# Kernel optimization log

Measured on AMD Instinct MI355X. Metric: run time of the kernel, lower is better.

Reference implementation:

```python
import jax, jax.numpy as jnp
import numpy as np

N = 8192          # number of nodes
E = 524288        # number of edges (avg degree 64)
D = 256           # latent_dim
NEG_FILL = -1e9   # torch.full fill value


def setup_inputs() -> dict:
    key = jax.random.key(0)
    k1, k2, k3, k4, k5, k6 = jax.random.split(key, 6)
    encoded = jax.random.normal(k1, (N, D), dtype=jnp.float32)
    h = jax.random.normal(k2, (N, D), dtype=jnp.float32)
    edge_index = jax.random.randint(k3, (2, E), 0, N, dtype=jnp.int64)
    edge_attr = jax.random.normal(k4, (E,), dtype=jnp.float32)
    # Linear weights (bias=False); stored as [in, out] for x @ W
    W1 = jax.random.normal(k5, (2 * D + 1, D), dtype=jnp.float32) * (1.0 / np.sqrt(2 * D + 1))
    W2 = jax.random.normal(k6, (D, 1), dtype=jnp.float32) * (1.0 / np.sqrt(D))
    return {"encoded": encoded, "h": h, "edge_index": edge_index,
            "edge_attr": edge_attr, "W1": W1, "W2": W2}


def reference(encoded, h, edge_index, edge_attr, W1, W2):
    left, right = edge_index[0], edge_index[1]
    # gather endpoint states and concat with scalar edge feature -> [E, 2D+1]
    feats = jnp.concatenate([h[left], h[right], edge_attr[:, None]], axis=1)
    # 2-layer MLP (no bias): Linear -> ReLU -> Linear -> [E]
    scores = (jax.nn.relu(feats @ W1) @ W2)[:, 0]
    # scatter into dense (N, N) matrix prefilled with -1e9
    result = jnp.full((h.shape[0], h.shape[0]), NEG_FILL, dtype=h.dtype)
    return result.at[left, right].set(scores)
```

## Files before the change

### kernel.cpp

```cpp
#include <hip/hip_runtime.h>

#define N_NODES 8192
#define E_EDGES 524288
#define D_DIM   256
#define NEG_FILL -1e9f

#define PROJ_BLOCKS 256
#define ROWS_PER_BLOCK 32
#define FILL_BLOCKS 1792

#define EDGE_BLOCKS 2048
#define EDGES_PER_WAVE 64

typedef float vfloat4 __attribute__((ext_vector_type(4)));
typedef float vfloat2 __attribute__((ext_vector_type(2)));

__global__ __launch_bounds__(256) void fill_proj_kernel(
    const float* __restrict__ h,
    const float* __restrict__ W1,
    float* __restrict__ out,
    unsigned char* __restrict__ AB)
{
    if (blockIdx.x < PROJ_BLOCKS) {
        __shared__ float hs[ROWS_PER_BLOCK * D_DIM];
        const int t  = threadIdx.x;
        const int r0 = blockIdx.x * ROWS_PER_BLOCK;
        const float* hp = h + (long long)r0 * D_DIM;
        for (int i = t; i < ROWS_PER_BLOCK * D_DIM; i += 256) hs[i] = hp[i];
        __syncthreads();

        float accA[ROWS_PER_BLOCK];
        float accB[ROWS_PER_BLOCK];
        #pragma unroll
        for (int r = 0; r < ROWS_PER_BLOCK; ++r) { accA[r] = 0.f; accB[r] = 0.f; }

        for (int k = 0; k < D_DIM; k += 4) {
            float wa0 = W1[(k + 0) * D_DIM + t];
            float wa1 = W1[(k + 1) * D_DIM + t];
            float wa2 = W1[(k + 2) * D_DIM + t];
            float wa3 = W1[(k + 3) * D_DIM + t];
            float wb0 = W1[(256 + k + 0) * D_DIM + t];
            float wb1 = W1[(256 + k + 1) * D_DIM + t];
            float wb2 = W1[(256 + k + 2) * D_DIM + t];
            float wb3 = W1[(256 + k + 3) * D_DIM + t];
            #pragma unroll
            for (int r = 0; r < ROWS_PER_BLOCK; ++r) {
                const float4 hv = *(const float4*)&hs[r * D_DIM + k];
                accA[r] = fmaf(hv.x, wa0, accA[r]);
                accA[r] = fmaf(hv.y, wa1, accA[r]);
                accA[r] = fmaf(hv.z, wa2, accA[r]);
                accA[r] = fmaf(hv.w, wa3, accA[r]);
                accB[r] = fmaf(hv.x, wb0, accB[r]);
                accB[r] = fmaf(hv.y, wb1, accB[r]);
                accB[r] = fmaf(hv.z, wb2, accB[r]);
                accB[r] = fmaf(hv.w, wb3, accB[r]);
            }
        }

        unsigned char* A = AB;
        unsigned char* B = AB + (long long)N_NODES * D_DIM;
        #pragma unroll
        for (int r = 0; r < ROWS_PER_BLOCK; ++r) {
            int pa = __builtin_amdgcn_cvt_pk_fp8_f32(accA[r], accA[r], 0, false);
            int pb = __builtin_amdgcn_cvt_pk_fp8_f32(accB[r], accB[r], 0, false);
            A[(long long)(r0 + r) * D_DIM + t] = (unsigned char)(pa & 0xFF);
            B[(long long)(r0 + r) * D_DIM + t] = (unsigned char)(pb & 0xFF);
        }
    } else {
        const int b = blockIdx.x - PROJ_BLOCKS;
        const int nvec = (N_NODES / 4) * N_NODES;
        vfloat4 fv = { NEG_FILL, NEG_FILL, NEG_FILL, NEG_FILL };
        vfloat4* o4 = (vfloat4*)out;
        for (int i = b * 256 + threadIdx.x; i < nvec; i += FILL_BLOCKS * 256)
            __builtin_nontemporal_store(fv, &o4[i]);
    }
}

__global__ __launch_bounds__(256) void edge_kernel(
    const int* __restrict__ eidx,
    const float* __restrict__ eattr,
    const float* __restrict__ W1,
    const float* __restrict__ W2,
    const unsigned char* __restrict__ AB,
    float* __restrict__ out)
{
    const int wave = blockIdx.x * 4 + (threadIdx.x >> 6);
    const int lane = threadIdx.x & 63;
    const int g    = lane >> 4;
    const int t    = lane & 15;
    const int base = wave * EDGES_PER_WAVE;

    const int   l_all = eidx[base + lane];
    const int   r_all = eidx[E_EDGES + base + lane];
    const float a_all = eattr[base + lane];

    const int j0 = t * 16;
    const float4 wl0 = *(const float4*)&W1[512 * D_DIM + j0 + 0];
    const float4 wl1 = *(const float4*)&W1[512 * D_DIM + j0 + 4];
    const float4 wl2 = *(const float4*)&W1[512 * D_DIM + j0 + 8];
    const float4 wl3 = *(const float4*)&W1[512 * D_DIM + j0 + 12];
    const float4 w20 = *(const float4*)&W2[j0 + 0];
    const float4 w21 = *(const float4*)&W2[j0 + 4];
    const float4 w22 = *(const float4*)&W2[j0 + 8];
    const float4 w23 = *(const float4*)&W2[j0 + 12];
    const unsigned char* Bt = AB + (long long)N_NODES * D_DIM;

    int   l_c  = __shfl(l_all, g);
    int   r_c  = __shfl(r_all, g);
    float at_c = __shfl(a_all, g);
    uint4 av_c = *(const uint4*)(AB + (unsigned)l_c * D_DIM + j0);
    uint4 bv_c = *(const uint4*)(Bt + (unsigned)r_c * D_DIM + j0);

    #pragma unroll 4
    for (int i = 0; i < EDGES_PER_WAVE / 4; ++i) {
        const int   l_cur = l_c;
        const int   r_cur = r_c;
        const float attr  = at_c;
        const uint4 av    = av_c;
        const uint4 bv    = bv_c;
        if (i + 1 < EDGES_PER_WAVE / 4) {
            l_c  = __shfl(l_all, 4 * (i + 1) + g);
            r_c  = __shfl(r_all, 4 * (i + 1) + g);
            at_c = __shfl(a_all, 4 * (i + 1) + g);
            av_c = *(const uint4*)(AB + (unsigned)l_c * D_DIM + j0);
            bv_c = *(const uint4*)(Bt + (unsigned)r_c * D_DIM + j0);
        }

        float s = 0.f;
        #define MLP_STEP(AV, BV, WL, W2V) {                                        \
            vfloat2 alo = __builtin_amdgcn_cvt_pk_f32_fp8((int)(AV), false);       \
            vfloat2 ahi = __builtin_amdgcn_cvt_pk_f32_fp8((int)(AV), true);        \
            vfloat2 blo = __builtin_amdgcn_cvt_pk_f32_fp8((int)(BV), false);       \
            vfloat2 bhi = __builtin_amdgcn_cvt_pk_f32_fp8((int)(BV), true);        \
            float hv;                                                              \
            hv = fmaf(attr, WL.x, alo.x + blo.x); hv = fmaxf(hv, 0.f); s = fmaf(hv, W2V.x, s); \
            hv = fmaf(attr, WL.y, alo.y + blo.y); hv = fmaxf(hv, 0.f); s = fmaf(hv, W2V.y, s); \
            hv = fmaf(attr, WL.z, ahi.x + bhi.x); hv = fmaxf(hv, 0.f); s = fmaf(hv, W2V.z, s); \
            hv = fmaf(attr, WL.w, ahi.y + bhi.y); hv = fmaxf(hv, 0.f); s = fmaf(hv, W2V.w, s); \
        }
        MLP_STEP(av.x, bv.x, wl0, w20);
        MLP_STEP(av.y, bv.y, wl1, w21);
        MLP_STEP(av.z, bv.z, wl2, w22);
        MLP_STEP(av.w, bv.w, wl3, w23);
        #undef MLP_STEP

        s += __shfl_xor(s, 8);
        s += __shfl_xor(s, 4);
        s += __shfl_xor(s, 2);
        s += __shfl_xor(s, 1);

        if (t == 0)
            __builtin_nontemporal_store(
                s, &out[(long long)l_cur * N_NODES + r_cur]);
    }
}

extern "C" void kernel_launch(void* const* d_in, const int* in_sizes, int n_in,
                              void* d_out, int out_size, void* d_ws, size_t ws_size,
                              hipStream_t stream) {
    const float* h     = (const float*)d_in[1];
    const int*   eidx  = (const int*)d_in[2];
    const float* eattr = (const float*)d_in[3];
    const float* W1    = (const float*)d_in[4];
    const float* W2    = (const float*)d_in[5];
    float* out = (float*)d_out;
    unsigned char* AB = (unsigned char*)d_ws;

    fill_proj_kernel<<<PROJ_BLOCKS + FILL_BLOCKS, 256, 0, stream>>>(h, W1, out, AB);
    edge_kernel<<<EDGE_BLOCKS, 256, 0, stream>>>(eidx, eattr, W1, W2, AB, out);
}
```

Baseline: 387.3 us.

## Bucket edges by source-row slab before scoring to localize scattered output writes

Adds a histogram over source-node slabs (32 rows each), built in the fill blocks, then a scan and an atomic-cursor permute that reorders edges by slab into packed (l<<16|r) and attribute arrays. The edge kernel reads the permuted edges and swizzles block IDs so concurrently running blocks touch different slabs. The aim is to make the scattered 4-byte output stores and A-row gathers more local in memory and cache. In exchange it adds a memset, two small kernels, global atomics and an extra pass over the edge arrays. It also relies on node IDs fitting in 16 bits.

After: 800.0 us. 107% more time.

```diff
diff --git a/kernel.cpp b/kernel.cpp
--- a/kernel.cpp
+++ b/kernel.cpp
@@ -8,25 +8,31 @@
 #define PROJ_BLOCKS 256
 #define ROWS_PER_BLOCK 32
 #define FILL_BLOCKS 1792
-
+#define NSLAB 256
+
+#define PERM_BLOCKS 1024
 #define EDGE_BLOCKS 2048
 #define EDGES_PER_WAVE 64
 
 typedef float vfloat4 __attribute__((ext_vector_type(4)));
 typedef float vfloat2 __attribute__((ext_vector_type(2)));
 
-__global__ __launch_bounds__(256) void fill_proj_kernel(
+__global__ __launch_bounds__(256) void fill_proj_hist_kernel(
     const float* __restrict__ h,
     const float* __restrict__ W1,
+    const int* __restrict__ eidx,
     float* __restrict__ out,
-    unsigned char* __restrict__ AB)
+    unsigned char* __restrict__ AB,
+    unsigned* __restrict__ hist)
 {
     if (blockIdx.x < PROJ_BLOCKS) {
         __shared__ float hs[ROWS_PER_BLOCK * D_DIM];
         const int t  = threadIdx.x;
         const int r0 = blockIdx.x * ROWS_PER_BLOCK;
-        const float* hp = h + (long long)r0 * D_DIM;
-        for (int i = t; i < ROWS_PER_BLOCK * D_DIM; i += 256) hs[i] = hp[i];
+        const vfloat4* hp4 = (const vfloat4*)(h + (long long)r0 * D_DIM);
+        vfloat4* hs4 = (vfloat4*)hs;
+        for (int i = t; i < ROWS_PER_BLOCK * D_DIM / 4; i += 256)
+            hs4[i] = __builtin_nontemporal_load(&hp4[i]);
         __syncthreads();
 
         float accA[ROWS_PER_BLOCK];
@@ -68,6 +74,10 @@
         }
     } else {
         const int b = blockIdx.x - PROJ_BLOCKS;
+        for (int i = b * 256 + threadIdx.x; i < E_EDGES; i += FILL_BLOCKS * 256) {
+            int l = __builtin_nontemporal_load(&eidx[i]);
+            atomicAdd(&hist[l >> 5], 1u);
+        }
         const int nvec = (N_NODES / 4) * N_NODES;
         vfloat4 fv = { NEG_FILL, NEG_FILL, NEG_FILL, NEG_FILL };
         vfloat4* o4 = (vfloat4*)out;
@@ -76,23 +86,58 @@
     }
 }
 
-__global__ __launch_bounds__(256) void edge_kernel(
+__global__ __launch_bounds__(NSLAB) void scan_kernel(
+    const unsigned* __restrict__ hist,
+    unsigned* __restrict__ cursor)
+{
+    __shared__ unsigned tmp[NSLAB];
+    const int t = threadIdx.x;
+    const unsigned v = hist[t];
+    tmp[t] = v;
+    __syncthreads();
+    for (int off = 1; off < NSLAB; off <<= 1) {
+        unsigned u = (t >= off) ? tmp[t - off] : 0u;
+        __syncthreads();
+        tmp[t] += u;
+        __syncthreads();
+    }
+    cursor[t] = tmp[t] - v;
+}
+
+__global__ __launch_bounds__(256) void permute_kernel(
     const int* __restrict__ eidx,
     const float* __restrict__ eattr,
+    unsigned* __restrict__ cursor,
+    unsigned* __restrict__ slr,
+    float* __restrict__ sat)
+{
+    for (int i = blockIdx.x * 256 + threadIdx.x; i < E_EDGES; i += PERM_BLOCKS * 256) {
+        const int   l = __builtin_nontemporal_load(&eidx[i]);
+        const int   r = __builtin_nontemporal_load(&eidx[E_EDGES + i]);
+        const float a = __builtin_nontemporal_load(&eattr[i]);
+        const unsigned pos = atomicAdd(&cursor[l >> 5], 1u);
+        __builtin_nontemporal_store(((unsigned)l << 16) | (unsigned)r, &slr[pos]);
+        __builtin_nontemporal_store(a, &sat[pos]);
+    }
+}
+
+__global__ __launch_bounds__(256) void edge_kernel(
+    const unsigned* __restrict__ slr,
+    const float* __restrict__ sat,
     const float* __restrict__ W1,
     const float* __restrict__ W2,
     const unsigned char* __restrict__ AB,
     float* __restrict__ out)
 {
-    const int wave = blockIdx.x * 4 + (threadIdx.x >> 6);
+    const int bid  = (blockIdx.x & 7) * (EDGE_BLOCKS / 8) + (blockIdx.x >> 3);
+    const int wave = bid * 4 + (threadIdx.x >> 6);
     const int lane = threadIdx.x & 63;
     const int g    = lane >> 4;
     const int t    = lane & 15;
-    const int base = wave * EDGES_PER_WAVE;
-
-    const int   l_all = eidx[base + lane];
-    const int   r_all = eidx[E_EDGES + base + lane];
-    const float a_all = eattr[base + lane];
+    const int ebase = wave * EDGES_PER_WAVE;
+
+    const unsigned lr_all = __builtin_nontemporal_load(&slr[ebase + lane]);
+    const float    a_all  = __builtin_nontemporal_load(&sat[ebase + lane]);
 
     const int j0 = t * 16;
     const float4 wl0 = *(const float4*)&W1[512 * D_DIM + j0 + 0];
@@ -105,9 +150,9 @@
     const float4 w23 = *(const float4*)&W2[j0 + 12];
     const unsigned char* Bt = AB + (long long)N_NODES * D_DIM;
 
-    int   l_c  = __shfl(l_all, g);
-    int   r_c  = __shfl(r_all, g);
-    float at_c = __shfl(a_all, g);
+    unsigned lr_c = (unsigned)__shfl((int)lr_all, g);
+    float    at_c = __shfl(a_all, g);
+    int l_c = (int)(lr_c >> 16), r_c = (int)(lr_c & 0xFFFFu);
     uint4 av_c = *(const uint4*)(AB + (unsigned)l_c * D_DIM + j0);
     uint4 bv_c = *(const uint4*)(Bt + (unsigned)r_c * D_DIM + j0);
 
@@ -119,9 +164,9 @@
         const uint4 av    = av_c;
         const uint4 bv    = bv_c;
         if (i + 1 < EDGES_PER_WAVE / 4) {
-            l_c  = __shfl(l_all, 4 * (i + 1) + g);
-            r_c  = __shfl(r_all, 4 * (i + 1) + g);
+            unsigned lr_n = (unsigned)__shfl((int)lr_all, 4 * (i + 1) + g);
             at_c = __shfl(a_all, 4 * (i + 1) + g);
+            l_c = (int)(lr_n >> 16); r_c = (int)(lr_n & 0xFFFFu);
             av_c = *(const uint4*)(AB + (unsigned)l_c * D_DIM + j0);
             bv_c = *(const uint4*)(Bt + (unsigned)r_c * D_DIM + j0);
         }
@@ -164,8 +209,16 @@
     const float* W1    = (const float*)d_in[4];
     const float* W2    = (const float*)d_in[5];
     float* out = (float*)d_out;
-    unsigned char* AB = (unsigned char*)d_ws;
-
-    fill_proj_kernel<<<PROJ_BLOCKS + FILL_BLOCKS, 256, 0, stream>>>(h, W1, out, AB);
-    edge_kernel<<<EDGE_BLOCKS, 256, 0, stream>>>(eidx, eattr, W1, W2, AB, out);
-}
+
+    unsigned char* AB     = (unsigned char*)d_ws;
+    unsigned*      slr    = (unsigned*)((char*)d_ws + (4u << 20));
+    float*         sat    = (float*)((char*)d_ws + (6u << 20));
+    unsigned*      hist   = (unsigned*)((char*)d_ws + (8u << 20));
+    unsigned*      cursor = hist + NSLAB;
+
+    (void)hipMemsetAsync(hist, 0, NSLAB * sizeof(unsigned), stream);
+    fill_proj_hist_kernel<<<PROJ_BLOCKS + FILL_BLOCKS, 256, 0, stream>>>(h, W1, eidx, out, AB, hist);
+    scan_kernel<<<1, NSLAB, 0, stream>>>(hist, cursor);
+    permute_kernel<<<PERM_BLOCKS, 256, 0, stream>>>(eidx, eattr, cursor, slr, sat);
+    edge_kernel<<<EDGE_BLOCKS, 256, 0, stream>>>(slr, sat, W1, W2, AB, out);
+}
```
